# Kernel tuning notes

Hardware: AMD Instinct MI355X
Metric: run time of the kernel (lower is better)

## Reference

```python
import jax, jax.numpy as jnp
import numpy as np

DIM = 256
D_INNER = 512   # dim * expansion_factor
D_STATE = 16
DT_RANK = 16    # max(16, dim // 16) == d_state (required by broadcast in selective_scan_ref)
BATCH = 4
SEQ_LEN = 4096


def setup_inputs() -> dict:
    key = jax.random.key(0)
    ks = jax.random.split(key, 6)
    x = jax.random.normal(ks[0], (BATCH, SEQ_LEN, DIM), dtype=jnp.float32)
    # learned parameters (conv weights are dead code in the original forward and omitted)
    x_proj = jax.random.normal(ks[1], (DIM, 2 * D_INNER), dtype=jnp.float32) * 0.02
    dt_proj = jax.random.normal(ks[2], (D_INNER, DT_RANK), dtype=jnp.float32) * 0.02
    # original init: A_log param = -log(arange(1, d_state+1)) repeated over d_inner
    A_log = jnp.broadcast_to(-jnp.log(jnp.arange(1, D_STATE + 1, dtype=jnp.float32)), (D_INNER, D_STATE))
    B_proj = jax.random.normal(ks[3], (D_INNER, DT_RANK), dtype=jnp.float32) * 0.02
    C_proj = jax.random.normal(ks[4], (D_INNER, DT_RANK), dtype=jnp.float32) * 0.02
    D = jnp.ones((D_INNER,), dtype=jnp.float32)
    out_proj = jax.random.normal(ks[5], (D_INNER, DIM), dtype=jnp.float32) * 0.02
    dt_proj_bias = jnp.ones((DT_RANK,), dtype=jnp.float32)
    return {"x": x, "x_proj": x_proj, "dt_proj": dt_proj, "A_log": A_log,
            "B_proj": B_proj, "C_proj": C_proj, "D": D, "out_proj": out_proj,
            "dt_proj_bias": dt_proj_bias}


def reference(x, x_proj, dt_proj, A_log, B_proj, C_proj, D, out_proj, dt_proj_bias):
    # x: (B, L, dim)
    x_z = x @ x_proj                                  # (B, L, 2*d_inner)
    xp, z = jnp.split(x_z, 2, axis=-1)                # each (B, L, d_inner)
    # NOTE: original computes a depthwise conv then discards it; x_conv = silu(x_proj_out)
    u = jax.nn.silu(xp)                               # (B, L, d_inner)
    dt = jax.nn.softplus(u @ dt_proj + dt_proj_bias)  # (B, L, dt_rank==d_state)
    Bm = u @ B_proj                                   # (B, L, d_state)
    Cm = u @ C_proj                                   # (B, L, d_state)
    A = -jnp.exp(A_log)                               # (d_inner, d_state)

    def step(h, inp):
        dt_t, B_t, C_t, u_t = inp                     # (B,S),(B,S),(B,S),(B,Din)
        dA = jnp.exp(dt_t[:, None, :] * A[None])      # (B, Din, S)
        dBu = (dt_t * B_t)[:, None, :] * u_t[:, :, None]  # (B, Din, S)
        h = dA * h + dBu                              # (B, Din, S)
        y = jnp.einsum('bds,bs->bd', h, C_t)          # (B, Din)
        return h, y

    h0 = jnp.zeros((x.shape[0], D_INNER, D_STATE), dtype=x.dtype)
    xs = (jnp.swapaxes(dt, 0, 1), jnp.swapaxes(Bm, 0, 1),
          jnp.swapaxes(Cm, 0, 1), jnp.swapaxes(u, 0, 1))
    _, ys = jax.lax.scan(step, h0, xs)                # ys: (L, B, Din)
    y = jnp.swapaxes(ys, 0, 1)                        # (B, L, Din)
    y = y + u * D                                     # skip connection
    y = y * jax.nn.silu(z)                            # gate
    return y @ out_proj                               # (B, L, dim)
```

## Files before the change

### kernel.cpp

```cpp
#include <hip/hip_runtime.h>
#include <math.h>

#define BATCH   4
#define SEQLEN  4096
#define NDIM    256
#define DINNER  512
#define DSTATE  16
#define M_ROWS  (BATCH*SEQLEN)
#define CHUNK   64
#define NCHUNK  (SEQLEN/CHUNK)

typedef _Float16 half8 __attribute__((ext_vector_type(8)));
typedef _Float16 half4 __attribute__((ext_vector_type(4)));
typedef float floatx4 __attribute__((ext_vector_type(4)));

__global__ __launch_bounds__(256)
void prep_all(const float* __restrict__ X, const float* __restrict__ Wx,
              const float* __restrict__ Wo, const float* __restrict__ Wdt,
              const float* __restrict__ Wb, const float* __restrict__ Wc,
              _Float16* __restrict__ Xh, _Float16* __restrict__ W1h,
              _Float16* __restrict__ W4h, _Float16* __restrict__ Wphi,
              _Float16* __restrict__ Wplo) {
    const int bid = blockIdx.x;
    const int tid = threadIdx.x;
    if (bid < 2048) {
        const int c = bid * 256 + tid;
        const int l15   = c & 15;
        const int q     = (c >> 4) & 3;
        const int kb    = (c >> 6) & 7;
        const int mtile = c >> 9;
        const int row = mtile * 16 + l15;
        const int col = kb * 32 + q * 8;
        const float4 v0 = *(const float4*)(X + (size_t)row * 256 + col);
        const float4 v1 = *(const float4*)(X + (size_t)row * 256 + col + 4);
        half8 h;
        h[0] = (_Float16)v0.x; h[1] = (_Float16)v0.y;
        h[2] = (_Float16)v0.z; h[3] = (_Float16)v0.w;
        h[4] = (_Float16)v1.x; h[5] = (_Float16)v1.y;
        h[6] = (_Float16)v1.z; h[7] = (_Float16)v1.w;
        *(half8*)(Xh + (size_t)c * 8) = h;
    } else if (bid < 3072) {
        const int t = (bid - 2048) * 256 + tid;
        const int j  = t & 7;
        const int n  = (t >> 3) & 1023;
        const int q  = (t >> 13) & 3;
        const int kb = t >> 15;
        const int k  = kb * 32 + q * 8 + j;
        W1h[t] = (_Float16)Wx[(size_t)k * 1024 + n];
    } else if (bid < 3584) {
        const int t = (bid - 3072) * 256 + tid;
        const int j  = t & 7;
        const int n  = (t >> 3) & 255;
        const int q  = (t >> 11) & 3;
        const int kb = t >> 13;
        const int k  = kb * 32 + q * 8 + j;
        W4h[t] = (_Float16)Wo[(size_t)k * 256 + n];
    } else {
        const int t = (bid - 3584) * 256 + tid;
        const int n  = (t >> 3) & 63;
        const int q  = (t >> 9) & 3;
        const int kb = t >> 11;
        const int k  = kb * 32 + q * 8 + (t & 7);
        float v;
        if      (n < 16) v = Wdt[(size_t)k * 16 + n];
        else if (n < 32) v = Wb [(size_t)k * 16 + (n - 16)];
        else if (n < 48) v = Wc [(size_t)k * 16 + (n - 32)];
        else             v = 0.f;
        const _Float16 hi = (_Float16)v;
        Wphi[t] = hi;
        Wplo[t] = (_Float16)(v - (float)hi);
    }
}

__global__ __launch_bounds__(256, 2)
void mfma_gemm1(const _Float16* __restrict__ Ah, const _Float16* __restrict__ Wh,
                _Float16* __restrict__ O1, _Float16* __restrict__ O2) {
    const int NT = 1024;
    const int bid = blockIdx.x;
    const int by = bid & 127;
    const int bx = bid >> 7;
    const int tid = threadIdx.x;
    const int lane = tid & 63;
    const int w  = tid >> 6;
    const int wm = w >> 1, wn = w & 1;
    const int n0 = bx * 128;
    const int m0 = by * 128;
    const int l15 = lane & 15, q = lane >> 4;

    floatx4 acc[4][4];
    const floatx4 zero = {0.f, 0.f, 0.f, 0.f};
    #pragma unroll
    for (int i = 0; i < 4; i++)
        #pragma unroll
        for (int j = 0; j < 4; j++) acc[i][j] = zero;

    const _Float16* aBase = Ah + (size_t)(by * 8 + wm * 4) * 4096 + q * 128 + l15 * 8;
    const _Float16* wBase = Wh + ((size_t)q * NT + n0 + wn * 64 + l15) * 8;

    half8 a0[4], b0[4], a1[4], b1[4];
    #pragma unroll
    for (int mt = 0; mt < 4; mt++)
        a0[mt] = *(const half8*)(aBase + mt * 4096);
    #pragma unroll
    for (int nt = 0; nt < 4; nt++)
        b0[nt] = *(const half8*)(wBase + nt * 128);

    #pragma unroll
    for (int kb = 0; kb < 8; kb += 2) {
        #pragma unroll
        for (int mt = 0; mt < 4; mt++)
            a1[mt] = *(const half8*)(aBase + mt * 4096 + (kb + 1) * 512);
        #pragma unroll
        for (int nt = 0; nt < 4; nt++)
            b1[nt] = *(const half8*)(wBase + (size_t)(kb + 1) * NT * 32 + nt * 128);
        #pragma unroll
        for (int mt = 0; mt < 4; mt++)
            #pragma unroll
            for (int nt = 0; nt < 4; nt++)
                acc[mt][nt] = __builtin_amdgcn_mfma_f32_16x16x32_f16(
                    a0[mt], b0[nt], acc[mt][nt], 0, 0, 0);
        if (kb + 2 < 8) {
            #pragma unroll
            for (int mt = 0; mt < 4; mt++)
                a0[mt] = *(const half8*)(aBase + mt * 4096 + (kb + 2) * 512);
            #pragma unroll
            for (int nt = 0; nt < 4; nt++)
                b0[nt] = *(const half8*)(wBase + (size_t)(kb + 2) * NT * 32 + nt * 128);
        }
        #pragma unroll
        for (int mt = 0; mt < 4; mt++)
            #pragma unroll
            for (int nt = 0; nt < 4; nt++)
                acc[mt][nt] = __builtin_amdgcn_mfma_f32_16x16x32_f16(
                    a1[mt], b1[nt], acc[mt][nt], 0, 0, 0);
    }
    #pragma unroll
    for (int mt = 0; mt < 4; mt++) {
        #pragma unroll
        for (int nt = 0; nt < 4; nt++) {
            const int col = n0 + wn * 64 + nt * 16 + l15;
            #pragma unroll
            for (int r = 0; r < 4; r++) {
                const int row = m0 + wm * 64 + mt * 16 + q * 4 + r;
                float v = acc[mt][nt][r];
                v = v / (1.f + __expf(-v));
                if (col < DINNER) O1[(size_t)row * DINNER + col] = (_Float16)v;
                else              O2[(size_t)row * DINNER + col - DINNER] = (_Float16)v;
            }
        }
    }
}

__global__ __launch_bounds__(256, 2)
void mfma_gemm4(const _Float16* __restrict__ Ah, const _Float16* __restrict__ Wh,
                float* __restrict__ Out) {
    const int NT = 256;
    const int bid = blockIdx.x;
    const int by = bid & 127;
    const int bx = bid >> 7;
    const int tid = threadIdx.x;
    const int lane = tid & 63;
    const int w  = tid >> 6;
    const int wm = w >> 1, wn = w & 1;
    const int n0 = bx * 64;
    const int m0 = by * 128;
    const int l15 = lane & 15, q = lane >> 4;

    floatx4 acc[4][2];
    const floatx4 zero = {0.f, 0.f, 0.f, 0.f};
    #pragma unroll
    for (int i = 0; i < 4; i++)
        #pragma unroll
        for (int j = 0; j < 2; j++) acc[i][j] = zero;

    const _Float16* aBase = Ah + (size_t)(by * 8 + wm * 4) * 8192 + q * 128 + l15 * 8;
    const _Float16* wBase = Wh + ((size_t)q * NT + n0 + wn * 32 + l15) * 8;

    half8 a0[4], b0[2], a1[4], b1[2];
    #pragma unroll
    for (int mt = 0; mt < 4; mt++)
        a0[mt] = *(const half8*)(aBase + mt * 8192);
    #pragma unroll
    for (int nt = 0; nt < 2; nt++)
        b0[nt] = *(const half8*)(wBase + nt * 128);

    #pragma unroll
    for (int kb = 0; kb < 16; kb += 2) {
        #pragma unroll
        for (int mt = 0; mt < 4; mt++)
            a1[mt] = *(const half8*)(aBase + mt * 8192 + (kb + 1) * 512);
        #pragma unroll
        for (int nt = 0; nt < 2; nt++)
            b1[nt] = *(const half8*)(wBase + (size_t)(kb + 1) * NT * 32 + nt * 128);
        #pragma unroll
        for (int mt = 0; mt < 4; mt++)
            #pragma unroll
            for (int nt = 0; nt < 2; nt++)
                acc[mt][nt] = __builtin_amdgcn_mfma_f32_16x16x32_f16(
                    a0[mt], b0[nt], acc[mt][nt], 0, 0, 0);
        if (kb + 2 < 16) {
            #pragma unroll
            for (int mt = 0; mt < 4; mt++)
                a0[mt] = *(const half8*)(aBase + mt * 8192 + (kb + 2) * 512);
            #pragma unroll
            for (int nt = 0; nt < 2; nt++)
                b0[nt] = *(const half8*)(wBase + (size_t)(kb + 2) * NT * 32 + nt * 128);
        }
        #pragma unroll
        for (int mt = 0; mt < 4; mt++)
            #pragma unroll
            for (int nt = 0; nt < 2; nt++)
                acc[mt][nt] = __builtin_amdgcn_mfma_f32_16x16x32_f16(
                    a1[mt], b1[nt], acc[mt][nt], 0, 0, 0);
    }
    #pragma unroll
    for (int mt = 0; mt < 4; mt++) {
        #pragma unroll
        for (int nt = 0; nt < 2; nt++) {
            const int col = n0 + wn * 32 + nt * 16 + l15;
            #pragma unroll
            for (int r = 0; r < 4; r++) {
                const int row = m0 + wm * 64 + mt * 16 + q * 4 + r;
                Out[(size_t)row * NT + col] = acc[mt][nt][r];
            }
        }
    }
}

__global__ __launch_bounds__(256)
void proj_mfma(const _Float16* __restrict__ Uh,
               const _Float16* __restrict__ Whi, const _Float16* __restrict__ Wlo,
               const float* __restrict__ bias,
               float* __restrict__ DT, float* __restrict__ BM,
               float* __restrict__ CM) {
    const int tid = threadIdx.x;
    const int lane = tid & 63;
    const int w  = tid >> 6;
    const int wm = w >> 1, wn = w & 1;
    const int m0 = blockIdx.x * 64;
    const int l15 = lane & 15, q = lane >> 4;

    floatx4 acc[2][2];
    const floatx4 zero = {0.f, 0.f, 0.f, 0.f};
    #pragma unroll
    for (int i = 0; i < 2; i++)
        #pragma unroll
        for (int j = 0; j < 2; j++) acc[i][j] = zero;

    const _Float16* aBase = Uh + (size_t)(m0 + wm * 32 + l15) * DINNER + q * 8;

    for (int kb = 0; kb < DINNER / 32; kb++) {
        half8 bh[2], bl[2], a[2];
        #pragma unroll
        for (int mt = 0; mt < 2; mt++)
            a[mt] = *(const half8*)(aBase + (size_t)(mt * 16) * DINNER + kb * 32);
        #pragma unroll
        for (int nt = 0; nt < 2; nt++) {
            const size_t off =
                ((size_t)((kb * 4 + q) * 64) + wn * 32 + nt * 16 + l15) * 8;
            bh[nt] = *(const half8*)(Whi + off);
            bl[nt] = *(const half8*)(Wlo + off);
        }
        #pragma unroll
        for (int mt = 0; mt < 2; mt++)
            #pragma unroll
            for (int nt = 0; nt < 2; nt++) {
                acc[mt][nt] = __builtin_amdgcn_mfma_f32_16x16x32_f16(
                    a[mt], bh[nt], acc[mt][nt], 0, 0, 0);
                acc[mt][nt] = __builtin_amdgcn_mfma_f32_16x16x32_f16(
                    a[mt], bl[nt], acc[mt][nt], 0, 0, 0);
            }
    }
    #pragma unroll
    for (int mt = 0; mt < 2; mt++) {
        #pragma unroll
        for (int nt = 0; nt < 2; nt++) {
            const int col = wn * 32 + nt * 16 + l15;
            #pragma unroll
            for (int r = 0; r < 4; r++) {
                const int row = m0 + wm * 32 + mt * 16 + q * 4 + r;
                float v = acc[mt][nt][r];
                if (col < 16) {
                    float dv = v + bias[col];
                    dv = (dv > 20.f) ? dv : log1pf(__expf(dv));
                    DT[(size_t)row * 16 + col] = dv;
                } else if (col < 32) {
                    BM[(size_t)row * 16 + (col - 16)] = v;
                } else if (col < 48) {
                    CM[(size_t)row * 16 + (col - 32)] = v;
                }
            }
        }
    }
}

__global__ __launch_bounds__(256)
void scan_phase_a(const float* __restrict__ DT, const float* __restrict__ BM,
                  const _Float16* __restrict__ Uh,
                  const float* __restrict__ Alog,
                  float* __restrict__ HEND, float* __restrict__ PPROD) {
    __shared__ floatx4 sdt4[CHUNK * 4];
    __shared__ floatx4 sdb4[CHUNK * 4];
    const int tid = threadIdx.x;
    const int chunk = blockIdx.x;
    const int dg = blockIdx.y;
    const int b  = blockIdx.z;
    const int d  = dg*256 + tid;
    const int l0 = chunk * CHUNK;
    {
        const floatx4 dtv = ((const floatx4*)(DT + (size_t)(b*SEQLEN + l0)*16))[tid];
        const floatx4 bmv = ((const floatx4*)(BM + (size_t)(b*SEQLEN + l0)*16))[tid];
        sdt4[tid] = dtv;
        sdb4[tid] = dtv * bmv;
    }
    __syncthreads();
    floatx4 A4[4];
    #pragma unroll
    for (int qq = 0; qq < 4; qq++) {
        const floatx4 av = ((const floatx4*)(Alog + (size_t)d*16))[qq];
        A4[qq].x = -__expf(av.x); A4[qq].y = -__expf(av.y);
        A4[qq].z = -__expf(av.z); A4[qq].w = -__expf(av.w);
    }
    floatx4 h4[4], P4[4];
    #pragma unroll
    for (int qq = 0; qq < 4; qq++) {
        h4[qq] = (floatx4){0.f, 0.f, 0.f, 0.f};
        P4[qq] = (floatx4){1.f, 1.f, 1.f, 1.f};
    }
    const _Float16* uhp = Uh + ((size_t)(b*SEQLEN + l0))*DINNER + d;
    #pragma unroll 4
    for (int l = 0; l < CHUNK; l++) {
        const float u = (float)uhp[(size_t)l*DINNER];
        #pragma unroll
        for (int qq = 0; qq < 4; qq++) {
            const floatx4 dtv = sdt4[l*4 + qq];
            const floatx4 dbv = sdb4[l*4 + qq];
            floatx4 dA;
            dA.x = __expf(dtv.x * A4[qq].x);
            dA.y = __expf(dtv.y * A4[qq].y);
            dA.z = __expf(dtv.z * A4[qq].z);
            dA.w = __expf(dtv.w * A4[qq].w);
            h4[qq] = dA * h4[qq] + dbv * u;
            P4[qq] *= dA;
        }
    }
    floatx4* he = (floatx4*)(HEND  + ((size_t)(b*NCHUNK + chunk)*DINNER + d)*16);
    floatx4* pp = (floatx4*)(PPROD + ((size_t)(b*NCHUNK + chunk)*DINNER + d)*16);
    #pragma unroll
    for (int qq = 0; qq < 4; qq++) {
        he[qq] = h4[qq];
        pp[qq] = P4[qq];
    }
}

__global__ __launch_bounds__(256)
void scan_phase_b(const float* __restrict__ HEND, const float* __restrict__ PPROD,
                  float* __restrict__ H0) {
    const int tid = threadIdx.x;
    const int s  = tid & 15;
    const int dl = tid >> 4;
    const int blk = blockIdx.x;
    const int b  = blk >> 5;
    const int dg = blk & 31;
    const int d  = dg*16 + dl;
    float h = 0.f;
    for (int c0 = 0; c0 < NCHUNK; c0 += 8) {
        float Pv[8], Hv[8];
        #pragma unroll
        for (int j = 0; j < 8; j++) {
            const size_t idx = ((size_t)(b*NCHUNK + c0 + j)*DINNER + d)*16 + s;
            Pv[j] = PPROD[idx];
            Hv[j] = HEND [idx];
        }
        #pragma unroll
        for (int j = 0; j < 8; j++) {
            H0[((size_t)(b*NCHUNK + c0 + j)*DINNER + d)*16 + s] = h;
            h = Pv[j]*h + Hv[j];
        }
    }
}

__global__ __launch_bounds__(256)
void scan_phase_c(const float* __restrict__ DT, const float* __restrict__ BM,
                  const float* __restrict__ CM,
                  const _Float16* __restrict__ Uh, const _Float16* __restrict__ Gh,
                  const float* __restrict__ Alog,
                  const float* __restrict__ Dvec, const float* __restrict__ H0,
                  _Float16* __restrict__ Y2) {
    __shared__ floatx4 sdt4[CHUNK * 4];
    __shared__ floatx4 sdb4[CHUNK * 4];
    __shared__ floatx4 sc4 [CHUNK * 4];
    const int tid = threadIdx.x;
    const int chunk = blockIdx.x;
    const int dg = blockIdx.y;
    const int b  = blockIdx.z;
    const int d  = dg*256 + tid;
    const int l0 = chunk * CHUNK;
    {
        const floatx4 dtv = ((const floatx4*)(DT + (size_t)(b*SEQLEN + l0)*16))[tid];
        const floatx4 bmv = ((const floatx4*)(BM + (size_t)(b*SEQLEN + l0)*16))[tid];
        sdt4[tid] = dtv;
        sdb4[tid] = dtv * bmv;
        sc4 [tid] = ((const floatx4*)(CM + (size_t)(b*SEQLEN + l0)*16))[tid];
    }
    __syncthreads();
    floatx4 A4[4];
    #pragma unroll
    for (int qq = 0; qq < 4; qq++) {
        const floatx4 av = ((const floatx4*)(Alog + (size_t)d*16))[qq];
        A4[qq].x = -__expf(av.x); A4[qq].y = -__expf(av.y);
        A4[qq].z = -__expf(av.z); A4[qq].w = -__expf(av.w);
    }
    floatx4 h4[4];
    {
        const floatx4* h0 = (const floatx4*)(H0 +
            ((size_t)(b*NCHUNK + chunk)*DINNER + d)*16);
        #pragma unroll
        for (int qq = 0; qq < 4; qq++) h4[qq] = h0[qq];
    }
    const float Dd = Dvec[d];
    const size_t base = ((size_t)(b*SEQLEN + l0))*DINNER + d;
    const _Float16* uhp = Uh + base;
    const _Float16* ghp = Gh + base;
    const int mbase = b*SEQLEN + l0;
    const int kpart = (d >> 5) * 512 + ((d >> 3) & 3) * 128 + (d & 7);
    _Float16* yp2 = Y2 + (size_t)(mbase >> 4) * 8192 + kpart;
    #pragma unroll 4
    for (int l = 0; l < CHUNK; l++) {
        const float u = (float)uhp[(size_t)l*DINNER];
        const float g = (float)ghp[(size_t)l*DINNER];
        floatx4 y4 = {0.f, 0.f, 0.f, 0.f};
        #pragma unroll
        for (int qq = 0; qq < 4; qq++) {
            const floatx4 dtv = sdt4[l*4 + qq];
            const floatx4 dbv = sdb4[l*4 + qq];
            const floatx4 cv  = sc4 [l*4 + qq];
            floatx4 dA;
            dA.x = __expf(dtv.x * A4[qq].x);
            dA.y = __expf(dtv.y * A4[qq].y);
            dA.z = __expf(dtv.z * A4[qq].z);
            dA.w = __expf(dtv.w * A4[qq].w);
            h4[qq] = dA * h4[qq] + dbv * u;
            y4 += h4[qq] * cv;
        }
        const float y = y4.x + y4.y + y4.z + y4.w;
        yp2[(size_t)(l >> 4) * 8192 + (l & 15) * 8] =
            (_Float16)((y + u*Dd) * g);
    }
}

extern "C" void kernel_launch(void* const* d_in, const int* in_sizes, int n_in,
                              void* d_out, int out_size, void* d_ws, size_t ws_size,
                              hipStream_t stream) {
    const float* x        = (const float*)d_in[0];
    const float* x_proj   = (const float*)d_in[1];
    const float* dt_proj  = (const float*)d_in[2];
    const float* A_log    = (const float*)d_in[3];
    const float* B_proj   = (const float*)d_in[4];
    const float* C_proj   = (const float*)d_in[5];
    const float* Dvec     = (const float*)d_in[6];
    const float* out_proj = (const float*)d_in[7];
    const float* dt_bias  = (const float*)d_in[8];
    float* out = (float*)d_out;

    float* ws = (float*)d_ws;
    float* DT   = ws;
    float* BM   = DT   + (size_t)M_ROWS*DSTATE;
    float* CM   = BM   + (size_t)M_ROWS*DSTATE;
    float* HEND = CM   + (size_t)M_ROWS*DSTATE;
    float* PPRO = HEND + (size_t)BATCH*NCHUNK*DINNER*DSTATE;
    float* H0   = PPRO + (size_t)BATCH*NCHUNK*DINNER*DSTATE;
    _Float16* Y2   = (_Float16*)(H0 + (size_t)BATCH*NCHUNK*DINNER*DSTATE);
    _Float16* W1h  = Y2   + (size_t)M_ROWS*DINNER;
    _Float16* W4h  = W1h  + (size_t)NDIM*1024;
    _Float16* Wphi = W4h  + (size_t)DINNER*NDIM;
    _Float16* Wplo = Wphi + (size_t)32768;
    _Float16* Uh   = Wplo + (size_t)32768;
    _Float16* Gh   = Uh   + (size_t)M_ROWS*DINNER;
    _Float16* Xh   = Gh   + (size_t)M_ROWS*DINNER;
    (void)ws_size;

    prep_all<<<dim3(3712), 256, 0, stream>>>(x, x_proj, out_proj, dt_proj,
                                             B_proj, C_proj,
                                             Xh, W1h, W4h, Wphi, Wplo);
    mfma_gemm1<<<dim3(1024), 256, 0, stream>>>(Xh, W1h, Uh, Gh);
    proj_mfma<<<dim3(M_ROWS/64), 256, 0, stream>>>(Uh, Wphi, Wplo,
                                                   dt_bias, DT, BM, CM);
    scan_phase_a<<<dim3(NCHUNK, DINNER/256, BATCH), 256, 0, stream>>>(
        DT, BM, Uh, A_log, HEND, PPRO);
    scan_phase_b<<<dim3(128), 256, 0, stream>>>(HEND, PPRO, H0);
    scan_phase_c<<<dim3(NCHUNK, DINNER/256, BATCH), 256, 0, stream>>>(
        DT, BM, CM, Uh, Gh, A_log, Dvec, H0, Y2);
    mfma_gemm4<<<dim3(512), 256, 0, stream>>>(Y2, W4h, out);
}
```

Before: 200.9 us.

## Stage gemm1 operand tiles through LDS with async global-to-LDS double buffering

The first GEMM previously loaded A and W fragments straight from global memory into registers, so the two warps sharing a tile each fetched it separately. It now loads each k-slice of A and W into a double-buffered shared-memory tile using the global_load_lds builtin, with a barrier per k-step, and reads MFMA fragments from LDS. The goal is to remove redundant global traffic and cut register pressure, which is why occupancy is raised from 2 to 3 blocks per SM. The cost is 32KB of LDS per block and a barrier on every k iteration.

```diff
diff --git a/kernel.cpp b/kernel.cpp
--- a/kernel.cpp
+++ b/kernel.cpp
@@ -13,6 +13,12 @@
 typedef _Float16 half8 __attribute__((ext_vector_type(8)));
 typedef _Float16 half4 __attribute__((ext_vector_type(4)));
 typedef float floatx4 __attribute__((ext_vector_type(4)));
+
+__device__ __forceinline__ void gload16(const void* g, void* l) {
+    __builtin_amdgcn_global_load_lds(
+        (const __attribute__((address_space(1))) void*)g,
+        (__attribute__((address_space(3))) void*)l, 16, 0, 0);
+}
 
 __global__ __launch_bounds__(256)
 void prep_all(const float* __restrict__ X, const float* __restrict__ Wx,
@@ -72,9 +78,10 @@
     }
 }
 
-__global__ __launch_bounds__(256, 2)
+__global__ __launch_bounds__(256, 3)
 void mfma_gemm1(const _Float16* __restrict__ Ah, const _Float16* __restrict__ Wh,
                 _Float16* __restrict__ O1, _Float16* __restrict__ O2) {
+    __shared__ _Float16 lds[2][8192];
     const int NT = 1024;
     const int bid = blockIdx.x;
     const int by = bid & 127;
@@ -94,46 +101,56 @@
         #pragma unroll
         for (int j = 0; j < 4; j++) acc[i][j] = zero;
 
-    const _Float16* aBase = Ah + (size_t)(by * 8 + wm * 4) * 4096 + q * 128 + l15 * 8;
-    const _Float16* wBase = Wh + ((size_t)q * NT + n0 + wn * 64 + l15) * 8;
-
-    half8 a0[4], b0[4], a1[4], b1[4];
-    #pragma unroll
-    for (int mt = 0; mt < 4; mt++)
-        a0[mt] = *(const half8*)(aBase + mt * 4096);
-    #pragma unroll
-    for (int nt = 0; nt < 4; nt++)
-        b0[nt] = *(const half8*)(wBase + nt * 128);
-
-    #pragma unroll
-    for (int kb = 0; kb < 8; kb += 2) {
+    const _Float16* gsrc[4];
+    int ldst[4];
+    #pragma unroll
+    for (int j = 0; j < 4; j++) {
+        const int seg = w * 4 + j;
+        if (seg < 8) {
+            gsrc[j] = Ah + (size_t)(by * 8 + seg) * 4096 + (size_t)lane * 8;
+            ldst[j] = seg * 512;
+        } else {
+            const int s2 = seg - 8;
+            gsrc[j] = Wh + (size_t)(s2 >> 1) * NT * 8 + (size_t)n0 * 8
+                         + (size_t)(s2 & 1) * 512 + (size_t)lane * 8;
+            ldst[j] = 4096 + s2 * 512;
+        }
+    }
+    const size_t astep = 512;
+    const size_t bstep = (size_t)NT * 32;
+    const size_t kstep0 = (w * 4 < 8) ? astep : bstep;
+
+    #pragma unroll
+    for (int j = 0; j < 4; j++)
+        gload16(gsrc[j], &lds[0][ldst[j]]);
+    __syncthreads();
+
+    int bf = 0;
+    #pragma unroll
+    for (int kb = 0; kb < 8; kb++) {
+        if (kb + 1 < 8) {
+            #pragma unroll
+            for (int j = 0; j < 4; j++)
+                gload16(gsrc[j] + (size_t)(kb + 1) * kstep0, &lds[bf ^ 1][ldst[j]]);
+        }
+        half8 af[4], bfr[4];
         #pragma unroll
         for (int mt = 0; mt < 4; mt++)
-            a1[mt] = *(const half8*)(aBase + mt * 4096 + (kb + 1) * 512);
+            af[mt] = *(const half8*)&lds[bf][(wm * 4 + mt) * 512 + q * 128 + l15 * 8];
         #pragma unroll
         for (int nt = 0; nt < 4; nt++)
-            b1[nt] = *(const half8*)(wBase + (size_t)(kb + 1) * NT * 32 + nt * 128);
+            bfr[nt] = *(const half8*)&lds[bf][4096 + q * 1024
+                                              + (wn * 64 + nt * 16 + l15) * 8];
         #pragma unroll
         for (int mt = 0; mt < 4; mt++)
             #pragma unroll
             for (int nt = 0; nt < 4; nt++)
                 acc[mt][nt] = __builtin_amdgcn_mfma_f32_16x16x32_f16(
-                    a0[mt], b0[nt], acc[mt][nt], 0, 0, 0);
-        if (kb + 2 < 8) {
-            #pragma unroll
-            for (int mt = 0; mt < 4; mt++)
-                a0[mt] = *(const half8*)(aBase + mt * 4096 + (kb + 2) * 512);
-            #pragma unroll
-            for (int nt = 0; nt < 4; nt++)
-                b0[nt] = *(const half8*)(wBase + (size_t)(kb + 2) * NT * 32 + nt * 128);
-        }
-        #pragma unroll
-        for (int mt = 0; mt < 4; mt++)
-            #pragma unroll
-            for (int nt = 0; nt < 4; nt++)
-                acc[mt][nt] = __builtin_amdgcn_mfma_f32_16x16x32_f16(
-                    a1[mt], b1[nt], acc[mt][nt], 0, 0, 0);
-    }
+                    af[mt], bfr[nt], acc[mt][nt], 0, 0, 0);
+        __syncthreads();
+        bf ^= 1;
+    }
+
     #pragma unroll
     for (int mt = 0; mt < 4; mt++) {
         #pragma unroll
```

New measurement: 205.6 us. 1.02x slower.
